# Kernel optimization log

Measured on AMD Instinct MI355X. Metric: run time of the kernel, lower is better.

## Reference

```python
import jax, jax.numpy as jnp
import numpy as np
from jax import lax

STRIDE, PADDING, DILATION = 1, 1, 1


def setup_inputs() -> dict:
    key = jax.random.key(0)
    ks = jax.random.split(key, 6)
    B, C, H, W = 32, 128, 64, 64
    K, O, ksz = 4, 256, 3
    red = 32  # C // reduction
    # kaiming-ish scales
    return {
        "x": jax.random.normal(ks[0], (B, C, H, W), jnp.float32),
        "weights": jax.random.normal(ks[1], (K, O, C, ksz, ksz), jnp.float32) * (1.0 / np.sqrt(C * ksz * ksz)),
        "w1": jax.random.normal(ks[2], (red, C), jnp.float32) * (1.0 / np.sqrt(C)),
        "b1": jnp.zeros((red,), jnp.float32),
        "w2": jax.random.normal(ks[3], (K, red), jnp.float32) * (1.0 / np.sqrt(red)),
        "b2": jnp.zeros((K,), jnp.float32),
    }


def reference(x, weights, w1, b1, w2, b2):
    B, C, H, W = x.shape
    K, O, Cw, kh, kw = weights.shape
    # attention over kernels: global avg pool -> MLP -> softmax  [B, K]
    pooled = jnp.mean(x, axis=(2, 3))                       # [B, C]
    h = jax.nn.relu(pooled @ w1.T + b1)                     # [B, red]
    att = jax.nn.softmax(h @ w2.T + b2, axis=1)             # [B, K]
    # per-sample mixed kernel: [B, O, C, kh, kw]
    wk = jnp.einsum('bk,koihw->boihw', att, weights)
    # batched per-sample conv via grouped convolution (groups = B)
    lhs = x.reshape(1, B * C, H, W)
    rhs = wk.reshape(B * O, C, kh, kw)
    out = lax.conv_general_dilated(
        lhs, rhs,
        window_strides=(STRIDE, STRIDE),
        padding=[(PADDING, PADDING), (PADDING, PADDING)],
        rhs_dilation=(DILATION, DILATION),
        dimension_numbers=('NCHW', 'OIHW', 'NCHW'),
        feature_group_count=B,
    )
    Ho, Wo = out.shape[2], out.shape[3]
    return out.reshape(B, O, Ho, Wo)
```

## Files before the change

kernel.cpp:

```cpp
#include <hip/hip_runtime.h>
#include <math.h>

#define BB 32
#define CC 128
#define HH 64
#define WW 64
#define KK 4
#define OO 256
#define RED 32
#define HWSZ (HH*WW)
#define XT_W 66

typedef __attribute__((ext_vector_type(8))) short bf16x8;
typedef __attribute__((ext_vector_type(4))) float f32x4;

static __device__ __forceinline__ unsigned short f2bf(float f) {
    unsigned int u = __float_as_uint(f);
    u += 0x7FFF + ((u >> 16) & 1);
    return (unsigned short)(u >> 16);
}

__global__ __launch_bounds__(256) void transpose_pool(const float* __restrict__ x,
        unsigned short* __restrict__ xt, float* __restrict__ partial) {
    __shared__ float lt[CC][65];
    int h = blockIdx.x & 63;
    int b = blockIdx.x >> 6;
    const float* xb = x + ((size_t)b * CC * HH + h) * WW;
    for (int i = threadIdx.x; i < CC * 16; i += 256) {
        int c = i >> 4, f4 = i & 15;
        float4 v = *(const float4*)(xb + (size_t)c * HWSZ + f4 * 4);
        lt[c][f4 * 4 + 0] = v.x;
        lt[c][f4 * 4 + 1] = v.y;
        lt[c][f4 * 4 + 2] = v.z;
        lt[c][f4 * 4 + 3] = v.w;
    }
    __syncthreads();
    size_t rowbase = ((size_t)b * XT_W + (h + 1)) * XT_W;
    for (int i = threadIdx.x; i < 64 * 16; i += 256) {
        int ww = i >> 4, cs = i & 15;
        bf16x8 pk;
#pragma unroll
        for (int j = 0; j < 8; ++j) pk[j] = (short)f2bf(lt[cs * 8 + j][ww]);
        *(bf16x8*)&xt[(rowbase + (ww + 1)) * CC + cs * 8] = pk;
    }
    if (threadIdx.x < 32) {
        int cs = threadIdx.x & 15;
        int col = (threadIdx.x < 16) ? 0 : 65;
        *(f32x4*)&xt[(rowbase + col) * CC + cs * 8] = (f32x4){0.f, 0.f, 0.f, 0.f};
    }
    if (h == 0 || h == 63) {
        int hr = (h == 0) ? 0 : 65;
        size_t rb = ((size_t)b * XT_W + hr) * XT_W;
        for (int i = threadIdx.x; i < XT_W * 16; i += 256) {
            int px = i >> 4, cs = i & 15;
            *(f32x4*)&xt[(rb + px) * CC + cs * 8] = (f32x4){0.f, 0.f, 0.f, 0.f};
        }
    }
    if (threadIdx.x < CC) {
        float s = 0.f;
#pragma unroll
        for (int j = 0; j < WW; ++j) s += lt[threadIdx.x][j];
        partial[(size_t)blockIdx.x * CC + threadIdx.x] = s;
    }
}

__global__ void att_kernel(const float* __restrict__ partial,
        const float* __restrict__ w1, const float* __restrict__ b1,
        const float* __restrict__ w2, const float* __restrict__ b2,
        float* __restrict__ att) {
    int b = blockIdx.x;
    int tid = threadIdx.x;
    __shared__ float ps[CC];
    __shared__ float hs[RED];
    __shared__ float ls[KK];
    if (tid < CC) {
        const float* pp = partial + (size_t)b * HH * CC + tid;
        float s = 0.f;
#pragma unroll
        for (int h = 0; h < HH; ++h) s += pp[(size_t)h * CC];
        ps[tid] = s * (1.0f / (float)HWSZ);
    }
    __syncthreads();
    int r = tid >> 3, j = tid & 7;
    const float* w1r = w1 + r * CC + j * 16;
    float p = 0.f;
#pragma unroll
    for (int c = 0; c < 16; ++c) p = fmaf(ps[j * 16 + c], w1r[c], p);
    p += __shfl_xor(p, 1, 64);
    p += __shfl_xor(p, 2, 64);
    p += __shfl_xor(p, 4, 64);
    if (j == 0) hs[r] = fmaxf(p + b1[r], 0.f);
    __syncthreads();
    if (tid < KK) {
        float acc = b2[tid];
        const float* w2k = w2 + tid * RED;
#pragma unroll
        for (int rr = 0; rr < RED; ++rr) acc = fmaf(hs[rr], w2k[rr], acc);
        ls[tid] = acc;
    }
    __syncthreads();
    if (tid == 0) {
        float m = fmaxf(fmaxf(ls[0], ls[1]), fmaxf(ls[2], ls[3]));
        float e0 = expf(ls[0] - m), e1 = expf(ls[1] - m);
        float e2 = expf(ls[2] - m), e3 = expf(ls[3] - m);
        float inv = 1.0f / (e0 + e1 + e2 + e3);
        att[b * KK + 0] = e0 * inv; att[b * KK + 1] = e1 * inv;
        att[b * KK + 2] = e2 * inv; att[b * KK + 3] = e3 * inv;
    }
}

__global__ __launch_bounds__(256) void mix_kernel(const float* __restrict__ w,
        const float* __restrict__ att, unsigned short* __restrict__ wk) {
    int gid = blockIdx.x * 256 + threadIdx.x;
    int c = gid & 127;
    int o = (gid >> 7) & 255;
    int b = gid >> 15;
    float a[KK];
#pragma unroll
    for (int k = 0; k < KK; ++k) a[k] = att[b * KK + k];
    float mixed[9];
#pragma unroll
    for (int t = 0; t < 9; ++t) mixed[t] = 0.f;
#pragma unroll
    for (int k = 0; k < KK; ++k) {
        const float* p = w + (((size_t)k * OO + o) * CC + c) * 9;
#pragma unroll
        for (int t = 0; t < 9; ++t) mixed[t] = fmaf(a[k], p[t], mixed[t]);
    }
#pragma unroll
    for (int t = 0; t < 9; ++t)
        wk[(((size_t)b * 9 + t) * OO + o) * CC + c] = f2bf(mixed[t]);
}

#define XS_C 40
#define AL_C 40
__global__ __launch_bounds__(256, 2) void conv_mfma(const unsigned short* __restrict__ xt,
        const unsigned short* __restrict__ wk, float* __restrict__ out) {
    __shared__ unsigned short xs[6 * 66 * XS_C];
    __shared__ unsigned short als[2][128 * AL_C];

    int blk = blockIdx.x;
    int rg = blk & 15;
    int ot = (blk >> 4) & 1;
    int b  = blk >> 5;
    int r0 = rg * 4;
    int o0 = ot * 128;

    int tid = threadIdx.x;
    int lane = tid & 63;
    int wid = tid >> 6;
    int wm = wid & 1;
    int wn = wid >> 1;
    int l15 = lane & 15;
    int l4 = lane >> 4;

    f32x4 acc[4][8];
#pragma unroll
    for (int i = 0; i < 4; ++i)
#pragma unroll
        for (int j = 0; j < 8; ++j) acc[i][j] = (f32x4){0.f, 0.f, 0.f, 0.f};

    const unsigned short* xtb = xt + ((size_t)b * XT_W + r0) * XT_W * CC;
    const unsigned short* wk_base = wk + ((size_t)b * 9 * OO + o0) * CC;

    for (int c0 = 0; c0 < CC; c0 += 32) {
        __syncthreads();
        for (int i = tid; i < 1584; i += 256) {
            int pix = i >> 2, seg = i & 3;
            int row = pix / 66, col = pix - row * 66;
            f32x4 v = *(const f32x4*)(xtb + ((size_t)row * XT_W + col) * CC + c0 + seg * 8);
            *(f32x4*)&xs[(size_t)pix * XS_C + seg * 8] = v;
        }
        {
            int ch = tid;
#pragma unroll
            for (int rep = 0; rep < 2; ++rep, ch += 256) {
                int o = ch >> 2, seg = ch & 3;
                f32x4 v = *(const f32x4*)(wk_base + (size_t)o * CC + c0 + seg * 8);
                *(f32x4*)&als[0][o * AL_C + seg * 8] = v;
            }
        }
        __syncthreads();

        for (int t = 0; t < 9; ++t) {
            if (t < 8) {
                int tn = t + 1;
                int ch = tid;
#pragma unroll
                for (int rep = 0; rep < 2; ++rep, ch += 256) {
                    int o = ch >> 2, seg = ch & 3;
                    f32x4 v = *(const f32x4*)(wk_base + ((size_t)tn * OO + o) * CC + c0 + seg * 8);
                    *(f32x4*)&als[tn & 1][o * AL_C + seg * 8] = v;
                }
            }
            int kh = t / 3, kw = t - kh * 3;
            bf16x8 af[4], bfv[8];
#pragma unroll
            for (int mf = 0; mf < 4; ++mf)
                af[mf] = *(const bf16x8*)&als[t & 1][(wm * 64 + mf * 16 + l15) * AL_C + l4 * 8];
#pragma unroll
            for (int nf = 0; nf < 8; ++nf) {
                int prow = wn * 2 + (nf >> 2) + kh;
                int pcol = (nf & 3) * 16 + l15 + kw;
                bfv[nf] = *(const bf16x8*)&xs[(prow * 66 + pcol) * XS_C + l4 * 8];
            }
#pragma unroll
            for (int mf = 0; mf < 4; ++mf)
#pragma unroll
                for (int nf = 0; nf < 8; ++nf)
                    acc[mf][nf] = __builtin_amdgcn_mfma_f32_16x16x32_bf16(
                        af[mf], bfv[nf], acc[mf][nf], 0, 0, 0);
            if (t < 8) __syncthreads();
        }
    }

    float* outb = out + ((size_t)b * OO + o0) * HWSZ;
#pragma unroll
    for (int mf = 0; mf < 4; ++mf)
#pragma unroll
        for (int nf = 0; nf < 8; ++nf) {
            int row = r0 + wn * 2 + (nf >> 2);
            int col = (nf & 3) * 16 + l15;
#pragma unroll
            for (int r = 0; r < 4; ++r) {
                int o = wm * 64 + mf * 16 + l4 * 4 + r;
                outb[(size_t)o * HWSZ + row * WW + col] = acc[mf][nf][r];
            }
        }
}

extern "C" void kernel_launch(void* const* d_in, const int* in_sizes, int n_in,
                              void* d_out, int out_size, void* d_ws, size_t ws_size,
                              hipStream_t stream) {
    const float* x       = (const float*)d_in[0];
    const float* weights = (const float*)d_in[1];
    const float* w1      = (const float*)d_in[2];
    const float* b1      = (const float*)d_in[3];
    const float* w2      = (const float*)d_in[4];
    const float* b2      = (const float*)d_in[5];
    float* out = (float*)d_out;

    char* ws = (char*)d_ws;
    float* partial      = (float*)ws;
    float* att          = (float*)(ws + 1048576);
    unsigned short* wk  = (unsigned short*)(ws + 1048576 + 4096);
    unsigned short* xtp = (unsigned short*)(ws + 1048576 + 4096 + 18874368);

    transpose_pool<<<BB * HH, 256, 0, stream>>>(x, xtp, partial);
    att_kernel<<<BB, 256, 0, stream>>>(partial, w1, b1, w2, b2, att);
    mix_kernel<<<BB * OO * CC / 256, 256, 0, stream>>>(weights, att, wk);
    conv_mfma<<<BB * 2 * 16, 256, 0, stream>>>(xtp, wk, out);
}
```

Measured before the change: 295.0 us.

## Channel-group layout, async global-to-LDS loads, XOR swizzle, and block remap

Reorganizes xt and wk into channel groups of 32 so each conv chunk reads a contiguous plane. Global loads are replaced with direct global_load_lds async copies into LDS. The padded LDS strides become an XOR swizzle to avoid bank conflicts, and block indices are remapped for locality. This is meant to cut register staging and scattered global reads, but it relies on barriers to order the async loads and only 16-byte LDS direct writes.

```diff
diff --git a/kernel.cpp b/kernel.cpp
--- a/kernel.cpp
+++ b/kernel.cpp
@@ -10,6 +10,7 @@
 #define RED 32
 #define HWSZ (HH*WW)
 #define XT_W 66
+#define GPLANE (XT_W*XT_W)
 
 typedef __attribute__((ext_vector_type(8))) short bf16x8;
 typedef __attribute__((ext_vector_type(4))) float f32x4;
@@ -18,6 +19,12 @@
     unsigned int u = __float_as_uint(f);
     u += 0x7FFF + ((u >> 16) & 1);
     return (unsigned short)(u >> 16);
+}
+
+static __device__ __forceinline__ void async16(unsigned short* lds, const unsigned short* g) {
+    __builtin_amdgcn_global_load_lds(
+        (const __attribute__((address_space(1))) unsigned int*)g,
+        (__attribute__((address_space(3))) unsigned int*)lds, 16, 0, 0);
 }
 
 __global__ __launch_bounds__(256) void transpose_pool(const float* __restrict__ x,
@@ -35,25 +42,26 @@
         lt[c][f4 * 4 + 3] = v.w;
     }
     __syncthreads();
-    size_t rowbase = ((size_t)b * XT_W + (h + 1)) * XT_W;
+    size_t bg = (size_t)b * 4;
     for (int i = threadIdx.x; i < 64 * 16; i += 256) {
         int ww = i >> 4, cs = i & 15;
         bf16x8 pk;
 #pragma unroll
         for (int j = 0; j < 8; ++j) pk[j] = (short)f2bf(lt[cs * 8 + j][ww]);
-        *(bf16x8*)&xt[(rowbase + (ww + 1)) * CC + cs * 8] = pk;
+        *(bf16x8*)&xt[(((bg + (cs >> 2)) * XT_W + (h + 1)) * XT_W + (ww + 1)) * 32 + (cs & 3) * 8] = pk;
     }
     if (threadIdx.x < 32) {
         int cs = threadIdx.x & 15;
         int col = (threadIdx.x < 16) ? 0 : 65;
-        *(f32x4*)&xt[(rowbase + col) * CC + cs * 8] = (f32x4){0.f, 0.f, 0.f, 0.f};
+        *(f32x4*)&xt[(((bg + (cs >> 2)) * XT_W + (h + 1)) * XT_W + col) * 32 + (cs & 3) * 8] =
+            (f32x4){0.f, 0.f, 0.f, 0.f};
     }
     if (h == 0 || h == 63) {
         int hr = (h == 0) ? 0 : 65;
-        size_t rb = ((size_t)b * XT_W + hr) * XT_W;
         for (int i = threadIdx.x; i < XT_W * 16; i += 256) {
             int px = i >> 4, cs = i & 15;
-            *(f32x4*)&xt[(rb + px) * CC + cs * 8] = (f32x4){0.f, 0.f, 0.f, 0.f};
+            *(f32x4*)&xt[(((bg + (cs >> 2)) * XT_W + hr) * XT_W + px) * 32 + (cs & 3) * 8] =
+                (f32x4){0.f, 0.f, 0.f, 0.f};
         }
     }
     if (threadIdx.x < CC) {
@@ -127,22 +135,24 @@
 #pragma unroll
         for (int t = 0; t < 9; ++t) mixed[t] = fmaf(a[k], p[t], mixed[t]);
     }
+    size_t base = ((size_t)b * 4 + (c >> 5)) * 9;
 #pragma unroll
     for (int t = 0; t < 9; ++t)
-        wk[(((size_t)b * 9 + t) * OO + o) * CC + c] = f2bf(mixed[t]);
-}
-
-#define XS_C 40
-#define AL_C 40
+        wk[((base + t) * OO + o) * 32 + (c & 31)] = f2bf(mixed[t]);
+}
+
+#define XS_C 32
+#define AL_C 32
 __global__ __launch_bounds__(256, 2) void conv_mfma(const unsigned short* __restrict__ xt,
         const unsigned short* __restrict__ wk, float* __restrict__ out) {
-    __shared__ unsigned short xs[6 * 66 * XS_C];
+    __shared__ unsigned short xs[6 * XT_W * XS_C];
     __shared__ unsigned short als[2][128 * AL_C];
 
-    int blk = blockIdx.x;
-    int rg = blk & 15;
-    int ot = (blk >> 4) & 1;
+    int bid = blockIdx.x;
+    int blk = (bid & 7) * 128 + (bid >> 3);
     int b  = blk >> 5;
+    int rg = (blk >> 1) & 15;
+    int ot = blk & 1;
     int r0 = rg * 4;
     int o0 = ot * 128;
 
@@ -160,49 +170,53 @@
 #pragma unroll
         for (int j = 0; j < 8; ++j) acc[i][j] = (f32x4){0.f, 0.f, 0.f, 0.f};
 
-    const unsigned short* xtb = xt + ((size_t)b * XT_W + r0) * XT_W * CC;
-    const unsigned short* wk_base = wk + ((size_t)b * 9 * OO + o0) * CC;
-
-    for (int c0 = 0; c0 < CC; c0 += 32) {
+    const unsigned short* xt_b = xt + (size_t)b * 4 * GPLANE * 32;
+    const unsigned short* wk_b = wk + (size_t)b * 4 * 9 * OO * 32;
+
+    for (int g = 0; g < 4; ++g) {
         __syncthreads();
+        const unsigned short* xsrc = xt_b + ((size_t)g * GPLANE + r0 * XT_W) * 32;
         for (int i = tid; i < 1584; i += 256) {
             int pix = i >> 2, seg = i & 3;
-            int row = pix / 66, col = pix - row * 66;
-            f32x4 v = *(const f32x4*)(xtb + ((size_t)row * XT_W + col) * CC + c0 + seg * 8);
-            *(f32x4*)&xs[(size_t)pix * XS_C + seg * 8] = v;
-        }
+            int segg = seg ^ ((pix >> 1) & 3);
+            async16(xs + i * 8, xsrc + pix * 32 + segg * 8);
+        }
+        const unsigned short* wsrc = wk_b + ((size_t)g * 9 * OO + o0) * 32;
         {
             int ch = tid;
 #pragma unroll
             for (int rep = 0; rep < 2; ++rep, ch += 256) {
                 int o = ch >> 2, seg = ch & 3;
-                f32x4 v = *(const f32x4*)(wk_base + (size_t)o * CC + c0 + seg * 8);
-                *(f32x4*)&als[0][o * AL_C + seg * 8] = v;
+                int segg = seg ^ ((o >> 1) & 3);
+                async16(als[0] + ch * 8, wsrc + o * 32 + segg * 8);
             }
         }
         __syncthreads();
 
         for (int t = 0; t < 9; ++t) {
             if (t < 8) {
-                int tn = t + 1;
                 int ch = tid;
 #pragma unroll
                 for (int rep = 0; rep < 2; ++rep, ch += 256) {
                     int o = ch >> 2, seg = ch & 3;
-                    f32x4 v = *(const f32x4*)(wk_base + ((size_t)tn * OO + o) * CC + c0 + seg * 8);
-                    *(f32x4*)&als[tn & 1][o * AL_C + seg * 8] = v;
+                    int segg = seg ^ ((o >> 1) & 3);
+                    async16(als[(t + 1) & 1] + ch * 8,
+                            wsrc + ((size_t)(t + 1) * OO + o) * 32 + segg * 8);
                 }
             }
             int kh = t / 3, kw = t - kh * 3;
             bf16x8 af[4], bfv[8];
 #pragma unroll
-            for (int mf = 0; mf < 4; ++mf)
-                af[mf] = *(const bf16x8*)&als[t & 1][(wm * 64 + mf * 16 + l15) * AL_C + l4 * 8];
+            for (int mf = 0; mf < 4; ++mf) {
+                int orow = wm * 64 + mf * 16 + l15;
+                af[mf] = *(const bf16x8*)&als[t & 1][orow * AL_C + (l4 ^ ((orow >> 1) & 3)) * 8];
+            }
 #pragma unroll
             for (int nf = 0; nf < 8; ++nf) {
                 int prow = wn * 2 + (nf >> 2) + kh;
                 int pcol = (nf & 3) * 16 + l15 + kw;
-                bfv[nf] = *(const bf16x8*)&xs[(prow * 66 + pcol) * XS_C + l4 * 8];
+                int pix = prow * XT_W + pcol;
+                bfv[nf] = *(const bf16x8*)&xs[pix * XS_C + (l4 ^ ((pix >> 1) & 3)) * 8];
             }
 #pragma unroll
             for (int mf = 0; mf < 4; ++mf)
```

Result: faster. 272.1 us (-7.7%).
